# Optimization experiments

Measured on AMD Instinct MI355X. Metric: run time of the kernel, lower is better.

## Reference

```python
import jax, jax.numpy as jnp
import numpy as np

N = 100_000      # nodes
E0 = 1_600_000   # raw edges (avg degree 16)
D = 128          # input_dim
H = 8            # heads
C = 16           # out_channels per head (feat_dim // n_head)
F = H * C        # feat_dim = 128
NCLS = 40
SLOPE = 0.2      # LeakyReLU negative_slope


def setup_inputs() -> dict:
    key = jax.random.key(0)
    ks = jax.random.split(key, 16)

    def glorot(k, shape, fan_in, fan_out):
        lim = np.sqrt(6.0 / (fan_in + fan_out))
        return jax.random.uniform(k, shape, jnp.float32, -lim, lim)

    inp = {
        "x": jax.random.normal(ks[0], (N, D), jnp.float32),
        "edge_index": jax.random.randint(ks[1], (2, E0), 0, N, jnp.int32),
        "edge_weight": jax.random.uniform(ks[2], (E0,), jnp.float32),
        # layer 1 params
        "W1": glorot(ks[3], (D, F), D, F),
        "att_l1": glorot(ks[4], (1, H, C), C, C),
        "att_r1": glorot(ks[5], (1, H, C), C, C),
        "b1": jnp.zeros((F,), jnp.float32),
        # layer 2 params
        "W2": glorot(ks[6], (F, F), F, F),
        "att_l2": glorot(ks[7], (1, H, C), C, C),
        "att_r2": glorot(ks[8], (1, H, C), C, C),
        "b2": jnp.zeros((F,), jnp.float32),
        # classifier
        "Wc": glorot(ks[9], (F, NCLS), F, NCLS),
        "bc": jnp.zeros((NCLS,), jnp.float32),
    }
    return inp


def _gat_layer(x, src, dst, mask, W, att_l, att_r, b):
    # x: [N, Din] -> h: [N, H, C]
    h = (x @ W).reshape(-1, H, C)
    al = jnp.sum(h * att_l, axis=-1)   # [N, H]
    ar = jnp.sum(h * att_r, axis=-1)   # [N, H]
    # per-edge score: alpha_j(src) + alpha_i(dst), LeakyReLU
    e = al[src] + ar[dst]              # [E, H]
    e = jnp.where(e > 0, e, SLOPE * e)
    # destination-grouped stable softmax (masked self-loop dups excluded)
    m = jax.ops.segment_max(e, dst, num_segments=N)
    m = jnp.where(jnp.isfinite(m), m, 0.0)
    ex = jnp.exp(e - m[dst]) * mask[:, None]
    denom = jax.ops.segment_sum(ex, dst, num_segments=N)
    alpha = ex / jnp.maximum(denom[dst], 1e-16)   # [E, H]
    # message = x_j * alpha, scatter-add to dst
    msg = h[src] * alpha[..., None]               # [E, H, C]
    out = jax.ops.segment_sum(msg, dst, num_segments=N)
    return out.reshape(-1, F) + b                 # concat heads + bias


def _augment(edge_index, dtype):
    # remove self-loops (via mask) then add one self-loop per node
    src0, dst0 = edge_index[0], edge_index[1]
    loop = jnp.arange(N, dtype=edge_index.dtype)
    src = jnp.concatenate([src0, loop])
    dst = jnp.concatenate([dst0, loop])
    mask = jnp.concatenate([(src0 != dst0).astype(dtype), jnp.ones((N,), dtype)])
    return src, dst, mask


def reference(x, edge_index, edge_weight, W1, att_l1, att_r1, b1,
              W2, att_l2, att_r2, b2, Wc, bc):
    # edge_weight is accepted but unused, matching the torch forward
    src, dst, mask = _augment(edge_index, x.dtype)
    h = _gat_layer(x, src, dst, mask, W1, att_l1, att_r1, b1)
    h = jax.nn.elu(h)
    h = _gat_layer(h, src, dst, mask, W2, att_l2, att_r2, b2)
    h = jax.nn.elu(h)
    # eval mode: dropout is identity
    return h @ Wc + bc
```

## Files before the change

kernel.cpp:

```cpp
#include <hip/hip_runtime.h>
#include <hip/hip_bf16.h>
#include <math.h>

#define NN 100000
#define E_RAW 1600000
#define E_TOT 1700000
#define HEADS 8
#define CH 16
#define FDIM 128
#define NCLS 40
#define SLOPE 0.2f

typedef short bf16x8 __attribute__((ext_vector_type(8)));
typedef float f32x4  __attribute__((ext_vector_type(4)));

__device__ __forceinline__ float elu1(float v) { return v > 0.f ? v : expm1f(v); }

__device__ __forceinline__ unsigned short f2bf(float f) {
    unsigned int u = __float_as_uint(f);
    u += 0x7fffu + ((u >> 16) & 1u);
    return (unsigned short)(u >> 16);
}
__device__ __forceinline__ float bf2f(unsigned short h) {
    return __uint_as_float((unsigned int)h << 16);
}

__global__ __launch_bounds__(256) void prep_w(const float* __restrict__ W1,
                                              const float* __restrict__ W2,
                                              unsigned short* __restrict__ whi1,
                                              unsigned short* __restrict__ wlo1,
                                              unsigned short* __restrict__ whi2,
                                              unsigned short* __restrict__ wlo2) {
    int t = blockIdx.x * 256 + threadIdx.x;
    const float* W = (t < 16384) ? W1 : W2;
    unsigned short* hi = (t < 16384) ? whi1 : whi2;
    unsigned short* lo = (t < 16384) ? wlo1 : wlo2;
    int e = t & 16383;
    int k = e & 127, n = e >> 7;
    float v = W[k * 128 + n];
    unsigned short h = f2bf(v);
    float r = v - bf2f(h);
    hi[e] = h; lo[e] = f2bf(r);
}

__global__ __launch_bounds__(256) void gemm_mfma(const float* __restrict__ X,
                                                 const unsigned short* __restrict__ Whi,
                                                 const unsigned short* __restrict__ Wlo,
                                                 const float* __restrict__ attl,
                                                 const float* __restrict__ attr,
                                                 unsigned short* __restrict__ Hb,
                                                 float* __restrict__ AL,
                                                 float* __restrict__ AR) {
    const int lane = threadIdx.x & 63;
    const int w    = threadIdx.x >> 6;
    const int m16  = lane & 15;
    const int koct = lane >> 4;
    const int rowA = blockIdx.x * 64 + w * 16 + m16;
    const int rowAc = rowA < NN ? rowA : NN - 1;

    f32x4 acc[8];
    #pragma unroll
    for (int c = 0; c < 8; ++c) acc[c] = (f32x4){0.f, 0.f, 0.f, 0.f};

    #pragma unroll
    for (int ks = 0; ks < 4; ++ks) {
        const int k0 = ks * 32;
        const float* xp = X + (size_t)rowAc * 128 + k0 + koct * 8;
        float xv[8];
        *(float4*)&xv[0] = *(const float4*)xp;
        *(float4*)&xv[4] = *(const float4*)(xp + 4);
        bf16x8 ahi, alo;
        #pragma unroll
        for (int j = 0; j < 8; ++j) {
            unsigned short h = f2bf(xv[j]);
            ahi[j] = (short)h;
            alo[j] = (short)f2bf(xv[j] - bf2f(h));
        }
        #pragma unroll
        for (int cf = 0; cf < 8; ++cf) {
            const size_t boff = (size_t)(cf * 16 + m16) * 128 + k0 + koct * 8;
            bf16x8 bhi = *(const bf16x8*)(Whi + boff);
            bf16x8 blo = *(const bf16x8*)(Wlo + boff);
            acc[cf] = __builtin_amdgcn_mfma_f32_16x16x32_bf16(ahi, bhi, acc[cf], 0, 0, 0);
            acc[cf] = __builtin_amdgcn_mfma_f32_16x16x32_bf16(alo, bhi, acc[cf], 0, 0, 0);
            acc[cf] = __builtin_amdgcn_mfma_f32_16x16x32_bf16(ahi, blo, acc[cf], 0, 0, 0);
        }
    }

    const int orow0 = blockIdx.x * 64 + w * 16 + koct * 4;
    #pragma unroll
    for (int cf = 0; cf < 8; ++cf) {
        const float lwv = attl[cf * 16 + m16];
        const float rwv = attr[cf * 16 + m16];
        #pragma unroll
        for (int r = 0; r < 4; ++r) {
            const int orow = orow0 + r;
            if (orow < NN)
                Hb[(size_t)orow * 128 + cf * 16 + m16] = f2bf(acc[cf][r]);
            float pl = acc[cf][r] * lwv;
            float pr = acc[cf][r] * rwv;
            #pragma unroll
            for (int off = 1; off < 16; off <<= 1) {
                pl += __shfl_xor(pl, off);
                pr += __shfl_xor(pr, off);
            }
            if (m16 == 0 && orow < NN) {
                AL[orow * 8 + cf] = pl;
                AR[orow * 8 + cf] = pr;
            }
        }
    }
}

__global__ __launch_bounds__(256) void csr_init_cnt(int* __restrict__ cnt) {
    int i = blockIdx.x * 256 + threadIdx.x;
    if (i < NN) cnt[i] = 1;
}

__global__ __launch_bounds__(256) void csr_hist(const int* __restrict__ dst_a,
                                                int* __restrict__ cnt) {
    int e = blockIdx.x * 256 + threadIdx.x;
    if (e < E_RAW) atomicAdd(&cnt[dst_a[e]], 1);
}

__global__ __launch_bounds__(256) void scan_block(const int* __restrict__ cnt,
                                                  int* __restrict__ part,
                                                  int* __restrict__ bsum) {
    __shared__ int s[256];
    int i = blockIdx.x * 256 + threadIdx.x;
    int v = (i < NN) ? cnt[i] : 0;
    s[threadIdx.x] = v;
    __syncthreads();
    for (int off = 1; off < 256; off <<= 1) {
        int t = (threadIdx.x >= off) ? s[threadIdx.x - off] : 0;
        __syncthreads();
        s[threadIdx.x] += t;
        __syncthreads();
    }
    if (i < NN) part[i] = s[threadIdx.x] - v;
    if (threadIdx.x == 255) bsum[blockIdx.x] = s[255];
}

__global__ __launch_bounds__(512) void scan_partials(int* __restrict__ bsum, int nb) {
    __shared__ int s[512];
    int v = (threadIdx.x < nb) ? bsum[threadIdx.x] : 0;
    s[threadIdx.x] = v;
    __syncthreads();
    for (int off = 1; off < 512; off <<= 1) {
        int t = (threadIdx.x >= off) ? s[threadIdx.x - off] : 0;
        __syncthreads();
        s[threadIdx.x] += t;
        __syncthreads();
    }
    if (threadIdx.x < nb) bsum[threadIdx.x] = s[threadIdx.x] - v;
}

__global__ __launch_bounds__(256) void scan_add(const int* __restrict__ part,
                                                const int* __restrict__ bsum,
                                                int* __restrict__ roff,
                                                int* __restrict__ rpos) {
    int i = blockIdx.x * 256 + threadIdx.x;
    if (i < NN) {
        int v = part[i] + bsum[blockIdx.x];
        roff[i] = v; rpos[i] = v;
    }
    if (i == NN) roff[NN] = E_TOT;
}

__global__ __launch_bounds__(256) void csr_scatter(const int* __restrict__ src_a,
                                                   const int* __restrict__ dst_a,
                                                   int* __restrict__ rpos,
                                                   int* __restrict__ csr) {
    int e = blockIdx.x * 256 + threadIdx.x;
    if (e >= E_TOT) return;
    int s, d, flag;
    if (e < E_RAW) { s = src_a[e]; d = dst_a[e]; flag = (s == d); }
    else           { s = d = e - E_RAW; flag = 0; }
    int pos = atomicAdd(&rpos[d], 1);
    csr[pos] = s | (flag << 31);
}

__global__ __launch_bounds__(256) void gat_fused(const int* __restrict__ roff,
                                                 const int* __restrict__ csr,
                                                 const float* __restrict__ AL,
                                                 const float* __restrict__ AR,
                                                 const unsigned short* __restrict__ Hb,
                                                 const float* __restrict__ bias,
                                                 float* __restrict__ Out) {
    const int lane = threadIdx.x & 63;
    const int n = blockIdx.x * 4 + (threadIdx.x >> 6);
    const int r0 = roff[n], r1 = roff[n + 1];

    const int hd = lane >> 3;
    const int t  = lane & 7;
    const float ard = AR[n * 8 + hd];
    float m = -3e38f, den = 0.f;
    for (int j = r0 + t; j < r1; j += 8) {
        int sw = csr[j];
        int s = sw & 0x7fffffff;
        float ev = AL[s * 8 + hd] + ard;
        ev = fmaxf(ev, SLOPE * ev);
        float mn = fmaxf(m, ev);
        float add = (sw >= 0) ? __expf(ev - mn) : 0.f;
        den = fmaf(den, __expf(m - mn), add);
        m = mn;
    }
    #pragma unroll
    for (int off = 1; off < 8; off <<= 1) {
        float m2 = __shfl_xor(m, off), d2 = __shfl_xor(den, off);
        float mn = fmaxf(m, m2);
        den = den * __expf(m - mn) + d2 * __expf(m2 - mn);
        m = mn;
    }
    const float S = m + __logf(fmaxf(den, 1e-16f));

    const int ef = lane >> 3;
    const int fl = lane & 7;
    const float S_b  = __shfl(S,   fl * 8);
    const float ar_b = __shfl(ard, fl * 8);
    float4 a0 = make_float4(0.f,0.f,0.f,0.f), a1 = a0, a2 = a0, a3 = a0;
    for (int j = r0; j < r1; j += 8) {
        int jj = j + ef;
        if (jj < r1) {
            int sw = csr[jj];
            int s = sw & 0x7fffffff;
            float ev = AL[s * 8 + fl] + ar_b;
            ev = fmaxf(ev, SLOPE * ev);
            float alpha = (sw >= 0) ? __expf(ev - S_b) : 0.f;
            const unsigned short* hp = Hb + (size_t)s * 128 + fl * 16;
            const uint4 q0 = *(const uint4*)hp;
            const uint4 q1 = *(const uint4*)(hp + 8);
            a0.x = fmaf(__uint_as_float(q0.x << 16),          alpha, a0.x);
            a0.y = fmaf(__uint_as_float(q0.x & 0xffff0000u),  alpha, a0.y);
            a0.z = fmaf(__uint_as_float(q0.y << 16),          alpha, a0.z);
            a0.w = fmaf(__uint_as_float(q0.y & 0xffff0000u),  alpha, a0.w);
            a1.x = fmaf(__uint_as_float(q0.z << 16),          alpha, a1.x);
            a1.y = fmaf(__uint_as_float(q0.z & 0xffff0000u),  alpha, a1.y);
            a1.z = fmaf(__uint_as_float(q0.w << 16),          alpha, a1.z);
            a1.w = fmaf(__uint_as_float(q0.w & 0xffff0000u),  alpha, a1.w);
            a2.x = fmaf(__uint_as_float(q1.x << 16),          alpha, a2.x);
            a2.y = fmaf(__uint_as_float(q1.x & 0xffff0000u),  alpha, a2.y);
            a2.z = fmaf(__uint_as_float(q1.y << 16),          alpha, a2.z);
            a2.w = fmaf(__uint_as_float(q1.y & 0xffff0000u),  alpha, a2.w);
            a3.x = fmaf(__uint_as_float(q1.z << 16),          alpha, a3.x);
            a3.y = fmaf(__uint_as_float(q1.z & 0xffff0000u),  alpha, a3.y);
            a3.z = fmaf(__uint_as_float(q1.w << 16),          alpha, a3.z);
            a3.w = fmaf(__uint_as_float(q1.w & 0xffff0000u),  alpha, a3.w);
        }
    }
    #pragma unroll
    for (int off = 8; off < 64; off <<= 1) {
        a0.x += __shfl_xor(a0.x, off); a0.y += __shfl_xor(a0.y, off);
        a0.z += __shfl_xor(a0.z, off); a0.w += __shfl_xor(a0.w, off);
        a1.x += __shfl_xor(a1.x, off); a1.y += __shfl_xor(a1.y, off);
        a1.z += __shfl_xor(a1.z, off); a1.w += __shfl_xor(a1.w, off);
        a2.x += __shfl_xor(a2.x, off); a2.y += __shfl_xor(a2.y, off);
        a2.z += __shfl_xor(a2.z, off); a2.w += __shfl_xor(a2.w, off);
        a3.x += __shfl_xor(a3.x, off); a3.y += __shfl_xor(a3.y, off);
        a3.z += __shfl_xor(a3.z, off); a3.w += __shfl_xor(a3.w, off);
    }
    if (lane < 8) {
        const float4* bp = (const float4*)(bias + lane * 16);
        float4 b0 = bp[0], b1 = bp[1], b2 = bp[2], b3 = bp[3];
        a0.x = elu1(a0.x + b0.x); a0.y = elu1(a0.y + b0.y);
        a0.z = elu1(a0.z + b0.z); a0.w = elu1(a0.w + b0.w);
        a1.x = elu1(a1.x + b1.x); a1.y = elu1(a1.y + b1.y);
        a1.z = elu1(a1.z + b1.z); a1.w = elu1(a1.w + b1.w);
        a2.x = elu1(a2.x + b2.x); a2.y = elu1(a2.y + b2.y);
        a2.z = elu1(a2.z + b2.z); a2.w = elu1(a2.w + b2.w);
        a3.x = elu1(a3.x + b3.x); a3.y = elu1(a3.y + b3.y);
        a3.z = elu1(a3.z + b3.z); a3.w = elu1(a3.w + b3.w);
        float4* op = (float4*)(Out + (size_t)n * 128 + lane * 16);
        op[0] = a0; op[1] = a1; op[2] = a2; op[3] = a3;
    }
}

__global__ __launch_bounds__(256) void classifier(const float* __restrict__ X,
                                                  const float* __restrict__ Wc,
                                                  const float* __restrict__ bc,
                                                  float* __restrict__ Out) {
    __shared__ float ws[128 * NCLS];
    __shared__ float xs[32][132];
    for (int i = threadIdx.x; i < 128 * NCLS; i += 256) ws[i] = Wc[i];
    const int row0 = blockIdx.x << 5;
    for (int i = threadIdx.x; i < 32 * 128; i += 256) {
        int r = i >> 7, k = i & 127;
        xs[r][k] = X[(size_t)(row0 + r) * 128 + k];
    }
    __syncthreads();
    const int r  = threadIdx.x >> 3;
    const int c0 = (threadIdx.x & 7) * 5;
    float acc[5] = {0.f,0.f,0.f,0.f,0.f};
    for (int k = 0; k < 128; ++k) {
        float xv = xs[r][k];
        #pragma unroll
        for (int j = 0; j < 5; ++j)
            acc[j] = fmaf(xv, ws[k * NCLS + c0 + j], acc[j]);
    }
    #pragma unroll
    for (int j = 0; j < 5; ++j)
        Out[(size_t)(row0 + r) * NCLS + c0 + j] = acc[j] + bc[c0 + j];
}

extern "C" void kernel_launch(void* const* d_in, const int* in_sizes, int n_in,
                              void* d_out, int out_size, void* d_ws, size_t ws_size,
                              hipStream_t stream) {
    const float* x    = (const float*)d_in[0];
    const int*   ei   = (const int*)  d_in[1];
    const float* W1   = (const float*)d_in[3];
    const float* al1  = (const float*)d_in[4];
    const float* ar1  = (const float*)d_in[5];
    const float* b1   = (const float*)d_in[6];
    const float* W2   = (const float*)d_in[7];
    const float* al2  = (const float*)d_in[8];
    const float* ar2  = (const float*)d_in[9];
    const float* b2   = (const float*)d_in[10];
    const float* Wc   = (const float*)d_in[11];
    const float* bc   = (const float*)d_in[12];
    float* out = (float*)d_out;

    const int* src = ei;
    const int* dst = ei + E_RAW;

    char* ws = (char*)d_ws;
    unsigned short* hb = (unsigned short*)(ws);
    unsigned short* whi1 = (unsigned short*)(ws + 25600000UL);
    unsigned short* wlo1 = (unsigned short*)(ws + 25632768UL);
    unsigned short* whi2 = (unsigned short*)(ws + 25665536UL);
    unsigned short* wlo2 = (unsigned short*)(ws + 25698304UL);
    float* acc  = (float*)(ws + 51200000UL);
    float* AL   = (float*)(ws + 102400000UL);
    float* AR   = (float*)(ws + 105600000UL);
    int*   csr  = (int*)  (ws + 108800000UL);
    int*   cnt  = (int*)  (ws + 115600000UL);
    int*   roff = (int*)  (ws + 116000000UL);
    int*   rpos = (int*)  (ws + 116400004UL);
    int*   part = (int*)  (ws + 116800004UL);
    int*   bsum = (int*)  (ws + 117200004UL);

    const int NB_N    = (NN + 255) / 256;
    const int gRaw    = (E_RAW + 255) / 256;
    const int gTot    = (E_TOT + 255) / 256;
    const int gRows32 = NN / 32;
    const int gGemm   = (NN + 63) / 64;
    const int gGat    = NN / 4;

    prep_w<<<128, 256, 0, stream>>>(W1, W2, whi1, wlo1, whi2, wlo2);

    csr_init_cnt<<<NB_N, 256, 0, stream>>>(cnt);
    csr_hist<<<gRaw, 256, 0, stream>>>(dst, cnt);
    scan_block<<<NB_N, 256, 0, stream>>>(cnt, part, bsum);
    scan_partials<<<1, 512, 0, stream>>>(bsum, NB_N);
    scan_add<<<NB_N, 256, 0, stream>>>(part, bsum, roff, rpos);
    csr_scatter<<<gTot, 256, 0, stream>>>(src, dst, rpos, csr);

    gemm_mfma<<<gGemm, 256, 0, stream>>>(x, whi1, wlo1, al1, ar1, hb, AL, AR);
    gat_fused<<<gGat, 256, 0, stream>>>(roff, csr, AL, AR, hb, b1, acc);

    gemm_mfma<<<gGemm, 256, 0, stream>>>(acc, whi2, wlo2, al2, ar2, hb, AL, AR);
    gat_fused<<<gGat, 256, 0, stream>>>(roff, csr, AL, AR, hb, b2, acc);

    classifier<<<gRows32, 256, 0, stream>>>(acc, Wc, bc, out);
}
```

Measured before the change: 739.1 us.

## Build CSR via two-level bucket partition to localize scatter atomics

Replaces the single global-atomic CSR scatter with a bucketed scheme. Edges are first partitioned by destination into 196 buckets of 512 nodes, using shared-memory ranks and one global atomic per bucket per block, and staged in workspace. A per-bucket kernel then scatters each bucket, so the rpos atomics and csr writes hit a small, cache-resident range. Self-loops are written directly in scan_add. This adds extra kernels and a staging pass over the edges; bucket_scatter runs only 196 blocks, which may leave the GPU underused.

```diff
diff --git a/kernel.cpp b/kernel.cpp
--- a/kernel.cpp
+++ b/kernel.cpp
@@ -10,6 +10,8 @@
 #define FDIM 128
 #define NCLS 40
 #define SLOPE 0.2f
+#define NBKT 196
+#define BSH 9
 
 typedef short bf16x8 __attribute__((ext_vector_type(8)));
 typedef float f32x4  __attribute__((ext_vector_type(4)));
@@ -158,26 +160,103 @@
 __global__ __launch_bounds__(256) void scan_add(const int* __restrict__ part,
                                                 const int* __restrict__ bsum,
                                                 int* __restrict__ roff,
-                                                int* __restrict__ rpos) {
+                                                int* __restrict__ rpos,
+                                                int* __restrict__ csr) {
     int i = blockIdx.x * 256 + threadIdx.x;
     if (i < NN) {
         int v = part[i] + bsum[blockIdx.x];
-        roff[i] = v; rpos[i] = v;
+        roff[i] = v;
+        rpos[i] = v + 1;
+        csr[v] = i;
     }
     if (i == NN) roff[NN] = E_TOT;
 }
 
-__global__ __launch_bounds__(256) void csr_scatter(const int* __restrict__ src_a,
-                                                   const int* __restrict__ dst_a,
-                                                   int* __restrict__ rpos,
-                                                   int* __restrict__ csr) {
-    int e = blockIdx.x * 256 + threadIdx.x;
-    if (e >= E_TOT) return;
-    int s, d, flag;
-    if (e < E_RAW) { s = src_a[e]; d = dst_a[e]; flag = (s == d); }
-    else           { s = d = e - E_RAW; flag = 0; }
-    int pos = atomicAdd(&rpos[d], 1);
-    csr[pos] = s | (flag << 31);
+__global__ __launch_bounds__(256) void bkt_cnt(const int* __restrict__ cnt,
+                                               int* __restrict__ bktCnt) {
+    __shared__ int red[8];
+    const int b = blockIdx.x;
+    const int base = b << BSH;
+    int sum = 0;
+    for (int i = threadIdx.x; i < (1 << BSH); i += 256) {
+        int n = base + i;
+        if (n < NN) sum += cnt[n] - 1;
+    }
+    #pragma unroll
+    for (int off = 1; off < 64; off <<= 1) sum += __shfl_xor(sum, off);
+    if ((threadIdx.x & 63) == 0) red[threadIdx.x >> 6] = sum;
+    __syncthreads();
+    if (threadIdx.x == 0)
+        bktCnt[b] = red[0] + red[1] + red[2] + red[3];
+}
+
+__global__ __launch_bounds__(256) void bkt_scan(const int* __restrict__ bktCnt,
+                                                int* __restrict__ bktOff,
+                                                int* __restrict__ bpos) {
+    __shared__ int s[256];
+    int v = (threadIdx.x < NBKT) ? bktCnt[threadIdx.x] : 0;
+    s[threadIdx.x] = v;
+    __syncthreads();
+    for (int off = 1; off < 256; off <<= 1) {
+        int t = (threadIdx.x >= off) ? s[threadIdx.x - off] : 0;
+        __syncthreads();
+        s[threadIdx.x] += t;
+        __syncthreads();
+    }
+    if (threadIdx.x < NBKT) {
+        int e = s[threadIdx.x] - v;
+        bktOff[threadIdx.x] = e;
+        bpos[threadIdx.x]   = e;
+    }
+}
+
+__global__ __launch_bounds__(256) void bucket_stage(const int* __restrict__ src_a,
+                                                    const int* __restrict__ dst_a,
+                                                    int* __restrict__ bpos,
+                                                    uint2* __restrict__ stage) {
+    __shared__ int lcnt[NBKT];
+    __shared__ int lbase[NBKT];
+    for (int i = threadIdx.x; i < NBKT; i += 256) lcnt[i] = 0;
+    __syncthreads();
+    const int e0 = blockIdx.x * 4096 + threadIdx.x;
+    int sv[16], dv[16], rk[16];
+    #pragma unroll
+    for (int it = 0; it < 16; ++it) {
+        int e = e0 + it * 256;
+        if (e < E_RAW) {
+            sv[it] = src_a[e];
+            dv[it] = dst_a[e];
+            rk[it] = atomicAdd(&lcnt[dv[it] >> BSH], 1);
+        } else dv[it] = -1;
+    }
+    __syncthreads();
+    for (int i = threadIdx.x; i < NBKT; i += 256)
+        lbase[i] = atomicAdd(&bpos[i], lcnt[i]);
+    __syncthreads();
+    #pragma unroll
+    for (int it = 0; it < 16; ++it) {
+        if (dv[it] >= 0) {
+            int b = dv[it] >> BSH;
+            unsigned int flag = (sv[it] == dv[it]) ? 0x80000000u : 0u;
+            uint2 rec; rec.x = (unsigned int)sv[it] | flag; rec.y = (unsigned int)dv[it];
+            stage[lbase[b] + rk[it]] = rec;
+        }
+    }
+}
+
+__global__ __launch_bounds__(256) void bucket_scatter(const int* __restrict__ bktOff,
+                                                      const int* __restrict__ bpos,
+                                                      const uint2* __restrict__ stage,
+                                                      int* __restrict__ rpos,
+                                                      int* __restrict__ csr) {
+    const int b = blockIdx.x;
+    const int lo = bktOff[b], hi = bpos[b];
+    for (int i = lo + threadIdx.x; i < hi; i += 256) {
+        uint2 rec = stage[i];
+        int d = (int)rec.y;
+        int p = atomicAdd(&rpos[d], 1);
+        csr[p] = (int)rec.x;
+    }
 }
 
 __global__ __launch_bounds__(256) void gat_fused(const int* __restrict__ roff,
@@ -324,6 +403,7 @@
 
     char* ws = (char*)d_ws;
     unsigned short* hb = (unsigned short*)(ws);
+    uint2* stage = (uint2*)(ws);
     unsigned short* whi1 = (unsigned short*)(ws + 25600000UL);
     unsigned short* wlo1 = (unsigned short*)(ws + 25632768UL);
     unsigned short* whi2 = (unsigned short*)(ws + 25665536UL);
@@ -337,10 +417,13 @@
     int*   rpos = (int*)  (ws + 116400004UL);
     int*   part = (int*)  (ws + 116800004UL);
     int*   bsum = (int*)  (ws + 117200004UL);
+    int*   bktCnt = (int*)(ws + 117300000UL);
+    int*   bktOff = (int*)(ws + 117304000UL);
+    int*   bpos   = (int*)(ws + 117308000UL);
 
     const int NB_N    = (NN + 255) / 256;
     const int gRaw    = (E_RAW + 255) / 256;
-    const int gTot    = (E_TOT + 255) / 256;
+    const int gStage  = (E_RAW + 4095) / 4096;
     const int gRows32 = NN / 32;
     const int gGemm   = (NN + 63) / 64;
     const int gGat    = NN / 4;
@@ -351,8 +434,11 @@
     csr_hist<<<gRaw, 256, 0, stream>>>(dst, cnt);
     scan_block<<<NB_N, 256, 0, stream>>>(cnt, part, bsum);
     scan_partials<<<1, 512, 0, stream>>>(bsum, NB_N);
-    scan_add<<<NB_N, 256, 0, stream>>>(part, bsum, roff, rpos);
-    csr_scatter<<<gTot, 256, 0, stream>>>(src, dst, rpos, csr);
+    scan_add<<<NB_N, 256, 0, stream>>>(part, bsum, roff, rpos, csr);
+    bkt_cnt<<<NBKT, 256, 0, stream>>>(cnt, bktCnt);
+    bkt_scan<<<1, 256, 0, stream>>>(bktCnt, bktOff, bpos);
+    bucket_stage<<<gStage, 256, 0, stream>>>(src, dst, bpos, stage);
+    bucket_scatter<<<NBKT, 256, 0, stream>>>(bktOff, bpos, stage, rpos, csr);
 
     gemm_mfma<<<gGemm, 256, 0, stream>>>(x, whi1, wlo1, al1, ar1, hb, AL, AR);
     gat_fused<<<gGat, 256, 0, stream>>>(roff, csr, AL, AR, hb, b1, acc);
```

New measurement: 676.3 us. 1.09x faster.
